# Optimization experiments

Measured on AMD Instinct MI355X. Metric: run time of the kernel, lower is better.

## Reference

```python
import jax, jax.numpy as jnp
import numpy as np

N = 50000        # n_nodes
E = 1_600_000    # n_edges (avg degree 32)
IN = 128         # in_dim
H = 8            # num_heads
R = 16           # hidden_rank
D = 16           # out_dim (per head)
SCALE = float(np.sqrt(D))


def setup_inputs() -> dict:
    key = jax.random.key(0)
    k1, k2, k3, k4, k5, k6 = jax.random.split(key, 6)
    h = jax.random.normal(k1, (N, IN), jnp.float32)
    src = jax.random.randint(k2, (E,), 0, N, dtype=jnp.int32)
    dst = jax.random.randint(k3, (E,), 0, N, dtype=jnp.int32)
    s = 1.0 / np.sqrt(IN)  # kaiming-ish scale
    p = jax.random.normal(k4, (IN, H * R), jnp.float32) * s
    q = jax.random.normal(k5, (IN, H * R), jnp.float32) * s
    Wv = jax.random.normal(k6, (IN, H * D), jnp.float32) * s
    return {"h": h, "src": src, "dst": dst, "p": p, "q": q, "Wv": Wv}


def reference(h, src, dst, p, q, Wv):
    # global_attention_type == 'transform' -> atted = h
    K = (h @ q).reshape(N, H, R)   # K_h = atted @ _q
    Q = (h @ p).reshape(N, H, R)   # Q_h = h @ _p
    V = (h @ Wv).reshape(N, H, D)  # V_h = V(h), no bias
    # per-edge score: (K[src] * Q[dst]).sum(-1, keepdim), then scaled exp
    score = jnp.sum(K[src] * Q[dst], axis=-1, keepdims=True)   # [E, H, 1]
    score = jnp.exp(jnp.clip(score / SCALE, -5.0, 5.0))
    # scatter-sum into destination nodes
    wV = jax.ops.segment_sum(V[src] * score, dst, num_segments=N)  # [N, H, D]
    z = jax.ops.segment_sum(score, dst, num_segments=N)            # [N, H, 1]
    z = jnp.where(z == 0, jnp.float32(0.001), z)
    return wV / z
```

## Files before the change

kernel.cpp:

```cpp
#include <hip/hip_runtime.h>
#include <hip/hip_fp16.h>


#define HNODE 64
#define EPB   4096
#define BKT_SHIFT 7
#define BKT_CAP 5120
#define CHUNK 40

typedef _Float16 f16x8 __attribute__((ext_vector_type(8)));
typedef float    f32x4 __attribute__((ext_vector_type(4)));
typedef _Float16 hv2   __attribute__((ext_vector_type(2)));

__device__ __forceinline__ float fdot2(unsigned a, unsigned b, float c) {
#if __has_builtin(__builtin_amdgcn_fdot2)
    return __builtin_amdgcn_fdot2(__builtin_bit_cast(hv2, a),
                                  __builtin_bit_cast(hv2, b), c, false);
#else
    __half2 ah = *(__half2*)&a, bh = *(__half2*)&b;
    float2 af = __half22float2(ah), bf = __half22float2(bh);
    return c + af.x * bf.x + af.y * bf.y;
#endif
}

__device__ __forceinline__ float2 h2f(unsigned u) {
    __half2 hh = *(__half2*)&u;
    return __half22float2(hh);
}

__device__ __forceinline__ unsigned pack2(float a, float b) {
    __half2 hh = __floats2half2_rn(a, b);
    return *(unsigned*)&hh;
}

__global__ __launch_bounds__(256) void wt_convert_kernel(
    const float* __restrict__ Wq, const float* __restrict__ Wp,
    const float* __restrict__ Wv, __half* __restrict__ Wt)
{
    int o = blockIdx.x * 256 + threadIdx.x;
    int m = o >> 14, rem = o & 16383;
    int nn = rem >> 7, kk = rem & 127;
    const float* W = (m == 0) ? Wq : (m == 1) ? Wp : Wv;
    Wt[o] = __float2half(W[kk * 128 + nn]);
}

__global__ __launch_bounds__(256) void gemm_scatter_kernel(
    const float* __restrict__ h, const __half* __restrict__ Wt,
    unsigned* __restrict__ KV, __half* __restrict__ Q, int n,
    const int* __restrict__ src, const int* __restrict__ dst,
    unsigned* __restrict__ ebuf, int* __restrict__ cnts,
    int E, int nbkt, int nblk_e, int gemm_blocks)
{
    __shared__ __align__(16) char smem[39936];
    const int t = threadIdx.x;

    if ((int)blockIdx.x < gemm_blocks) {
        _Float16* ws = (_Float16*)smem;
        const int wid = t >> 6, lane = t & 63;
        const int node0 = blockIdx.x * HNODE;
        const int mrow = lane & 15, quad = lane >> 4;

        const int row = node0 + wid * 16 + mrow;
        const bool rowvalid = (row < n);
        const int rowc = rowvalid ? row : (n - 1);

        f16x8 hfr[4];
        #pragma unroll
        for (int s = 0; s < 4; s++) {
            const float4* hp = (const float4*)(h + (size_t)rowc * 128 + quad * 8 + 32 * s);
            float4 f0 = hp[0], f1 = hp[1];
            f16x8 a;
            a[0] = (_Float16)f0.x; a[1] = (_Float16)f0.y;
            a[2] = (_Float16)f0.z; a[3] = (_Float16)f0.w;
            a[4] = (_Float16)f1.x; a[5] = (_Float16)f1.y;
            a[6] = (_Float16)f1.z; a[7] = (_Float16)f1.w;
            hfr[s] = a;
        }

        f32x4 acc[3][8];
        #pragma unroll
        for (int m = 0; m < 3; m++)
            #pragma unroll
            for (int ct = 0; ct < 8; ct++) acc[m][ct] = (f32x4){0.f, 0.f, 0.f, 0.f};

        #pragma unroll
        for (int m = 0; m < 3; m++) {
            __syncthreads();
            {
                const uint4* wg = (const uint4*)(Wt + (size_t)m * 16384);
                #pragma unroll
                for (int i = 0; i < 8; i++) {
                    int idx = t * 8 + i;
                    int r = idx >> 4, seg = idx & 15;
                    *(uint4*)(ws + r * 136 + seg * 8) = wg[idx];
                }
            }
            __syncthreads();
            #pragma unroll
            for (int s = 0; s < 4; s++) {
                #pragma unroll
                for (int ct = 0; ct < 8; ct++) {
                    f16x8 a = *(const f16x8*)(ws + (ct * 16 + mrow) * 136 + quad * 8 + 32 * s);
                    acc[m][ct] = __builtin_amdgcn_mfma_f32_16x16x32_f16(a, hfr[s], acc[m][ct], 0, 0, 0);
                }
            }
        }

        if (rowvalid) {
            unsigned* kvrow = KV + (size_t)row * 128;
            __half*   qrow  = Q  + (size_t)row * 128;
            #pragma unroll
            for (int ct = 0; ct < 8; ct++) {
                int qd = ct * 4 + quad;
                uint4 ov;
                ov.x = pack2(acc[0][ct][0], acc[0][ct][1]);
                ov.y = pack2(acc[0][ct][2], acc[0][ct][3]);
                ov.z = pack2(acc[2][ct][0], acc[2][ct][1]);
                ov.w = pack2(acc[2][ct][2], acc[2][ct][3]);
                *(uint4*)(kvrow + 4 * qd) = ov;
                uint2 qv;
                qv.x = pack2(acc[1][ct][0], acc[1][ct][1]);
                qv.y = pack2(acc[1][ct][2], acc[1][ct][3]);
                *(uint2*)(qrow + 4 * qd) = qv;
            }
        }
    } else {
        unsigned long long* sorted = (unsigned long long*)smem;
        int* cnt  = (int*)(smem + 32768);
        int* lofs = (int*)(smem + 34816);
        int* ts   = (int*)(smem + 36864);
        int* tot_sh = (int*)(smem + 37888);

        int blk = blockIdx.x - gemm_blocks;
        for (int i = t; i < 512; i += 256) cnt[i] = 0;
        __syncthreads();

        int4 sv[4], dv[4], rk[4];
        int base = blk * EPB + t * 4;
        #pragma unroll
        for (int r = 0; r < 4; r++) {
            int i = base + r * 1024;
            if (i + 3 < E) {
                sv[r] = *(const int4*)(src + i);
                dv[r] = *(const int4*)(dst + i);
            } else {
                int tsrc[4], tdst[4];
                for (int k = 0; k < 4; k++) {
                    int j = i + k;
                    tsrc[k] = (j < E) ? src[j] : 0;
                    tdst[k] = (j < E) ? dst[j] : -1;
                }
                sv[r] = make_int4(tsrc[0], tsrc[1], tsrc[2], tsrc[3]);
                dv[r] = make_int4(tdst[0], tdst[1], tdst[2], tdst[3]);
            }
            rk[r].x = (dv[r].x >= 0) ? atomicAdd(&cnt[dv[r].x >> BKT_SHIFT], 1) : 0;
            rk[r].y = (dv[r].y >= 0) ? atomicAdd(&cnt[dv[r].y >> BKT_SHIFT], 1) : 0;
            rk[r].z = (dv[r].z >= 0) ? atomicAdd(&cnt[dv[r].z >> BKT_SHIFT], 1) : 0;
            rk[r].w = (dv[r].w >= 0) ? atomicAdd(&cnt[dv[r].w >> BKT_SHIFT], 1) : 0;
        }
        __syncthreads();

        for (int i = t; i < nbkt; i += 256)
            cnts[blk * 512 + i] = cnt[i];

        int c0 = cnt[2 * t], c1 = cnt[2 * t + 1];
        int ps = c0 + c1;
        ts[t] = ps; __syncthreads();
        for (int off = 1; off < 256; off <<= 1) {
            int x = ts[t];
            int y = (t >= off) ? ts[t - off] : 0;
            __syncthreads();
            ts[t] = x + y;
            __syncthreads();
        }
        int pbase = ts[t] - ps;
        lofs[2 * t] = pbase;
        lofs[2 * t + 1] = pbase + c0;
        if (t == 255) *tot_sh = ts[255];
        __syncthreads();

        #pragma unroll
        for (int r = 0; r < 4; r++) {
            int s, d;
            d = dv[r].x; if (d >= 0) { s = sv[r].x; sorted[lofs[d >> BKT_SHIFT] + rk[r].x] = ((unsigned long long)d << 18) | (unsigned)s; }
            d = dv[r].y; if (d >= 0) { s = sv[r].y; sorted[lofs[d >> BKT_SHIFT] + rk[r].y] = ((unsigned long long)d << 18) | (unsigned)s; }
            d = dv[r].z; if (d >= 0) { s = sv[r].z; sorted[lofs[d >> BKT_SHIFT] + rk[r].z] = ((unsigned long long)d << 18) | (unsigned)s; }
            d = dv[r].w; if (d >= 0) { s = sv[r].w; sorted[lofs[d >> BKT_SHIFT] + rk[r].w] = ((unsigned long long)d << 18) | (unsigned)s; }
        }
        __syncthreads();

        int tot = *tot_sh;
        #pragma unroll
        for (int j = 0; j < 16; j++) {
            int i = j * 256 + t;
            if (i < tot) {
                unsigned long long e = sorted[i];
                int d = (int)(e >> 18);
                int b = d >> BKT_SHIFT;
                int k = i - lofs[b];
                if (k < CHUNK)
                    ebuf[((size_t)b * nblk_e + blk) * CHUNK + k] =
                        ((unsigned)(d & 127) << 18) | (unsigned)(e & 0x3FFFFu);
            }
        }
    }
}

__global__ __launch_bounds__(512) void fine_scatter_kernel(
    const unsigned* __restrict__ ebuf, const int* __restrict__ cnts,
    int2* __restrict__ offs, int* __restrict__ csr, int N, int nblk_e, int nbkt)
{
    __shared__ int cval[512];
    __shared__ int cofs[512];
    __shared__ int ts[512];
    __shared__ int ldeg[128];
    __shared__ int lstart[129];
    __shared__ int tot_sh;
    __shared__ unsigned sedge[BKT_CAP];
    __shared__ unsigned short srank[BKT_CAP];
    __shared__ int lcsr[BKT_CAP];

    int b = blockIdx.x, t = threadIdx.x;
    int node_base = b << BKT_SHIFT;
    int seg0 = b * BKT_CAP;

    int c = (t < nblk_e) ? cnts[t * 512 + b] : 0;
    if (c > CHUNK) c = CHUNK;
    cval[t] = c;
    ts[t] = c;
    if (t < 128) ldeg[t] = 0;
    __syncthreads();
    for (int off = 1; off < 512; off <<= 1) {
        int x = ts[t];
        int y = (t >= off) ? ts[t - off] : 0;
        __syncthreads();
        ts[t] = x + y;
        __syncthreads();
    }
    cofs[t] = ts[t] - cval[t];
    if (t == 511) tot_sh = (ts[511] <= BKT_CAP) ? ts[511] : BKT_CAP;
    __syncthreads();

    for (int idx = t; idx < nblk_e * CHUNK; idx += 512) {
        int cc = idx / CHUNK, k = idx - cc * CHUNK;
        if (k < cval[cc]) {
            int pos = cofs[cc] + k;
            if (pos < BKT_CAP)
                sedge[pos] = ebuf[((size_t)b * nblk_e + cc) * CHUNK + k];
        }
    }
    __syncthreads();

    int tot = tot_sh;
    for (int i = t; i < tot; i += 512)
        srank[i] = (unsigned short)atomicAdd(&ldeg[sedge[i] >> 18], 1);
    __syncthreads();

    int mydeg = (t < 128) ? ldeg[t] : 0;
    if (t < 128) ts[t] = mydeg;
    __syncthreads();
    for (int off = 1; off < 128; off <<= 1) {
        int x = (t < 128) ? ts[t] : 0;
        int y = (t >= off && t < 128) ? ts[t - off] : 0;
        __syncthreads();
        if (t < 128) ts[t] = x + y;
        __syncthreads();
    }
    if (t < 128) {
        int lbeg = ts[t] - mydeg;
        lstart[t] = lbeg;
        int node = node_base + t;
        if (node < N) offs[node] = make_int2(seg0 + lbeg, seg0 + lbeg + mydeg);
    }
    if (t == 127) lstart[128] = ts[127];
    __syncthreads();

    for (int i = t; i < tot; i += 512) {
        unsigned v = sedge[i];
        lcsr[lstart[v >> 18] + srank[i]] = (int)(v & 0x3FFFFu);
    }
    __syncthreads();

    for (int i = t; i < tot; i += 512)
        csr[seg0 + i] = lcsr[i];
}

__global__ __launch_bounds__(256) void aggregate_kernel(
    const uint4* __restrict__ KV, const uint2* __restrict__ Qr,
    const int2* __restrict__ offs, const int* __restrict__ csr,
    float4* __restrict__ out, int n)
{
    int t = threadIdx.x;
    int node = blockIdx.x * 4 + (t >> 6);
    if (node >= n) return;
    int lane = t & 63;
    int l = lane & 31;
    int eh = lane >> 5;

    uint2 qq = Qr[(size_t)node * 32 + l];
    int2 be = offs[node];
    int beg = be.x, cnt = be.y - be.x;

    float4 accV = make_float4(0.f, 0.f, 0.f, 0.f);
    float accZ = 0.f;

    int chunkbase = 0;
    int myidx = (beg + lane < be.y) ? csr[beg + lane] : 0;

    uint4 kvA = make_uint4(0, 0, 0, 0), kvB = make_uint4(0, 0, 0, 0);
    if (cnt > 0) kvA = KV[(size_t)__shfl(myidx, eh, 64) * 32 + l];
    if (cnt > 2) kvB = KV[(size_t)__shfl(myidx, 2 + eh, 64) * 32 + l];

    for (int e = 0; e < cnt; e += 2) {
        uint4 nkv;
        bool more = (e + 4 < cnt);
        if (more) {
            int off = e + 4 - chunkbase;
            if (off == 64) {
                chunkbase += 64;
                myidx = (beg + chunkbase + lane < be.y) ? csr[beg + chunkbase + lane] : 0;
                off = 0;
            }
            nkv = KV[(size_t)__shfl(myidx, off + eh, 64) * 32 + l];
        }
        float p = fdot2(kvA.x, qq.x, fdot2(kvA.y, qq.y, 0.f));
        p += __shfl_xor(p, 1);
        p += __shfl_xor(p, 2);
        float x = fminf(fmaxf(p * 0.25f, -5.f), 5.f);
        float sc = (e + eh < cnt) ? __expf(x) : 0.f;
        accZ += sc;
        float2 va = h2f(kvA.z), vb = h2f(kvA.w);
        accV.x += sc * va.x; accV.y += sc * va.y;
        accV.z += sc * vb.x; accV.w += sc * vb.y;
        kvA = kvB;
        if (more) kvB = nkv;
    }

    accZ   += __shfl_xor(accZ, 32);
    accV.x += __shfl_xor(accV.x, 32);
    accV.y += __shfl_xor(accV.y, 32);
    accV.z += __shfl_xor(accV.z, 32);
    accV.w += __shfl_xor(accV.w, 32);

    if (lane < 32) {
        if (accZ == 0.f) accZ = 0.001f;
        float inv = 1.0f / accZ;
        out[(size_t)node * 32 + l] =
            make_float4(accV.x * inv, accV.y * inv, accV.z * inv, accV.w * inv);
    }
}


extern "C" void kernel_launch(void* const* d_in, const int* in_sizes, int n_in,
                              void* d_out, int out_size, void* d_ws, size_t ws_size,
                              hipStream_t stream)
{
    const float* h   = (const float*)d_in[0];
    const int*   src = (const int*)d_in[1];
    const int*   dst = (const int*)d_in[2];
    const float* p   = (const float*)d_in[3];
    const float* q   = (const float*)d_in[4];
    const float* wv  = (const float*)d_in[5];
    float* out = (float*)d_out;

    const int N = in_sizes[0] / 128;
    const int E = in_sizes[1];
    const int nbkt = (N + 127) >> BKT_SHIFT;
    const int nblk_e = (E + EPB - 1) / EPB;
    const int gemm_blocks = (N + HNODE - 1) / HNODE;

    unsigned* KV = (unsigned*)d_ws;
    __half* Qh   = (__half*)(KV + (size_t)N * 128);
    unsigned* ebuf = (unsigned*)(Qh + (size_t)N * 128);
    int* cnts    = (int*)(ebuf + (size_t)nbkt * nblk_e * CHUNK);
    int* csr     = cnts + (size_t)nblk_e * 512;
    int2* offs   = (int2*)(csr + (size_t)nbkt * BKT_CAP);
    __half* Wt   = (__half*)(offs + N);

    wt_convert_kernel<<<192, 256, 0, stream>>>(q, p, wv, Wt);

    gemm_scatter_kernel<<<gemm_blocks + nblk_e, 256, 0, stream>>>(
        h, Wt, KV, Qh, N, src, dst, ebuf, cnts, E, nbkt, nblk_e, gemm_blocks);

    fine_scatter_kernel<<<nbkt, 512, 0, stream>>>(ebuf, cnts, offs, csr, N, nblk_e, nbkt);

    aggregate_kernel<<<(N + 3) / 4, 256, 0, stream>>>(
        (const uint4*)KV, (const uint2*)Qh, offs, csr, (float4*)out, N);
}
```

Baseline: 250.8 us.

## Store K/V/Q head-major and split aggregation per head across blocks

The GEMM epilogue now writes KV and Q in a head-major layout ([head][node][16]) instead of node-major. The aggregation kernel launches one block group per head, so each wavefront handles one head of a node and processes 16 edges per step with 4 lanes per edge, reducing across lanes at the end. The aim is more parallelism and more gathers in flight per wave, with each head's data for all nodes contiguous to improve cache locality. The cost is that the CSR indices and offsets are re-read once per head, there is 8x more thread work per node, and each gather is only 32 bytes.

New measurement: 277.4 us. +10.6%, slower.

```diff
diff --git a/kernel.cpp b/kernel.cpp
--- a/kernel.cpp
+++ b/kernel.cpp
@@ -107,21 +107,18 @@
         }
 
         if (rowvalid) {
-            unsigned* kvrow = KV + (size_t)row * 128;
-            __half*   qrow  = Q  + (size_t)row * 128;
             #pragma unroll
             for (int ct = 0; ct < 8; ct++) {
-                int qd = ct * 4 + quad;
                 uint4 ov;
                 ov.x = pack2(acc[0][ct][0], acc[0][ct][1]);
                 ov.y = pack2(acc[0][ct][2], acc[0][ct][3]);
                 ov.z = pack2(acc[2][ct][0], acc[2][ct][1]);
                 ov.w = pack2(acc[2][ct][2], acc[2][ct][3]);
-                *(uint4*)(kvrow + 4 * qd) = ov;
+                *(uint4*)(KV + (((size_t)ct * n + row) << 4) + 4 * quad) = ov;
                 uint2 qv;
                 qv.x = pack2(acc[1][ct][0], acc[1][ct][1]);
                 qv.y = pack2(acc[1][ct][2], acc[1][ct][3]);
-                *(uint2*)(qrow + 4 * qd) = qv;
+                *(uint2*)(Q + (((size_t)ct * n + row) << 4) + 4 * quad) = qv;
             }
         }
     } else {
@@ -286,18 +283,21 @@
 }
 
 __global__ __launch_bounds__(256) void aggregate_kernel(
-    const uint4* __restrict__ KV, const uint2* __restrict__ Qr,
+    const uint4* __restrict__ KVh,
+    const uint2* __restrict__ Qh,
     const int2* __restrict__ offs, const int* __restrict__ csr,
     float4* __restrict__ out, int n)
 {
     int t = threadIdx.x;
-    int node = blockIdx.x * 4 + (t >> 6);
+    int head = blockIdx.x & 7;
+    int node = (blockIdx.x >> 3) * 4 + (t >> 6);
     if (node >= n) return;
     int lane = t & 63;
-    int l = lane & 31;
-    int eh = lane >> 5;
-
-    uint2 qq = Qr[(size_t)node * 32 + l];
+    int c  = lane & 3;
+    int eh = lane >> 2;
+
+    size_t hn = (size_t)head * n;
+    uint2 qq = Qh[(hn + node) * 4 + c];
     int2 be = offs[node];
     int beg = be.x, cnt = be.y - be.x;
 
@@ -307,21 +307,21 @@
     int chunkbase = 0;
     int myidx = (beg + lane < be.y) ? csr[beg + lane] : 0;
 
-    uint4 kvA = make_uint4(0, 0, 0, 0), kvB = make_uint4(0, 0, 0, 0);
-    if (cnt > 0) kvA = KV[(size_t)__shfl(myidx, eh, 64) * 32 + l];
-    if (cnt > 2) kvB = KV[(size_t)__shfl(myidx, 2 + eh, 64) * 32 + l];
-
-    for (int e = 0; e < cnt; e += 2) {
+    uint4 kvA = make_uint4(0, 0, 0, 0);
+    if (cnt > 0)
+        kvA = KVh[(hn + (size_t)__shfl(myidx, eh, 64)) * 4 + c];
+
+    for (int e = 0; e < cnt; e += 16) {
         uint4 nkv;
-        bool more = (e + 4 < cnt);
+        bool more = (e + 16 < cnt);
         if (more) {
-            int off = e + 4 - chunkbase;
+            int off = e + 16 - chunkbase;
             if (off == 64) {
                 chunkbase += 64;
                 myidx = (beg + chunkbase + lane < be.y) ? csr[beg + chunkbase + lane] : 0;
                 off = 0;
             }
-            nkv = KV[(size_t)__shfl(myidx, off + eh, 64) * 32 + l];
+            nkv = KVh[(hn + (size_t)__shfl(myidx, off + eh, 64)) * 4 + c];
         }
         float p = fdot2(kvA.x, qq.x, fdot2(kvA.y, qq.y, 0.f));
         p += __shfl_xor(p, 1);
@@ -332,20 +332,22 @@
         float2 va = h2f(kvA.z), vb = h2f(kvA.w);
         accV.x += sc * va.x; accV.y += sc * va.y;
         accV.z += sc * vb.x; accV.w += sc * vb.y;
-        kvA = kvB;
-        if (more) kvB = nkv;
-    }
-
-    accZ   += __shfl_xor(accZ, 32);
-    accV.x += __shfl_xor(accV.x, 32);
-    accV.y += __shfl_xor(accV.y, 32);
-    accV.z += __shfl_xor(accV.z, 32);
-    accV.w += __shfl_xor(accV.w, 32);
-
-    if (lane < 32) {
+        if (more) kvA = nkv;
+    }
+
+    #pragma unroll
+    for (int m = 4; m <= 32; m <<= 1) {
+        accZ   += __shfl_xor(accZ, m);
+        accV.x += __shfl_xor(accV.x, m);
+        accV.y += __shfl_xor(accV.y, m);
+        accV.z += __shfl_xor(accV.z, m);
+        accV.w += __shfl_xor(accV.w, m);
+    }
+
+    if (lane < 4) {
         if (accZ == 0.f) accZ = 0.001f;
         float inv = 1.0f / accZ;
-        out[(size_t)node * 32 + l] =
+        out[(size_t)node * 32 + head * 4 + c] =
             make_float4(accV.x * inv, accV.y * inv, accV.z * inv, accV.w * inv);
     }
 }
@@ -384,6 +386,6 @@
 
     fine_scatter_kernel<<<nbkt, 512, 0, stream>>>(ebuf, cnts, offs, csr, N, nblk_e, nbkt);
 
-    aggregate_kernel<<<(N + 3) / 4, 256, 0, stream>>>(
+    aggregate_kernel<<<((N + 3) / 4) * 8, 256, 0, stream>>>(
         (const uint4*)KV, (const uint2*)Qh, offs, csr, (float4*)out, N);
 }
```
